# Performance work log

Hardware: AMD Instinct MI355X
Metric: run time of the kernel (lower is better)

## Reference

```python
import jax, jax.numpy as jnp
import numpy as np
import math

B, S, D = 4, 1024, 4096
H, KVH, HD = 32, 8, 128  # n_heads, n_kv_heads, dim_per_head
MAXB, MAXS = 4, 4096
START_POS = 1024


def setup_inputs() -> dict:
    key = jax.random.key(0)
    ks = jax.random.split(key, 7)
    scale = 0.02
    return {
        "x": jax.random.normal(ks[0], (B, S, D), dtype=jnp.float32),
        "wq": jax.random.normal(ks[1], (D, H * HD), dtype=jnp.float32) * scale,
        "wk": jax.random.normal(ks[2], (D, KVH * HD), dtype=jnp.float32) * scale,
        "wv": jax.random.normal(ks[3], (D, KVH * HD), dtype=jnp.float32) * scale,
        "wo": jax.random.normal(ks[4], (H * HD, D), dtype=jnp.float32) * scale,
        # cache positions [0, START_POS) hold previous context k/v
        "cache_k": jax.random.normal(ks[5], (MAXB, MAXS, KVH, HD), dtype=jnp.float32),
        "cache_v": jax.random.normal(ks[6], (MAXB, MAXS, KVH, HD), dtype=jnp.float32),
        "start_pos": START_POS,
    }


def _apply_rope(t, start_pos):
    # t: [B, S, n_heads, HD]; rotate interleaved (even, odd) pairs.
    hd = t.shape[-1]
    inv_freq = 1.0 / (10000.0 ** (jnp.arange(0, hd, 2, dtype=jnp.float32) / hd))
    m = jnp.arange(start_pos, start_pos + t.shape[1], dtype=jnp.float32)
    freqs = m[:, None] * inv_freq[None, :]              # [S, HD/2]
    cos = jnp.cos(freqs)[None, :, None, :]
    sin = jnp.sin(freqs)[None, :, None, :]
    tr = t.astype(jnp.float32).reshape(*t.shape[:-1], hd // 2, 2)
    a, b = tr[..., 0], tr[..., 1]
    out = jnp.stack([a * cos - b * sin, a * sin + b * cos], axis=-1)
    out = out.reshape(t.shape).astype(t.dtype)
    # original torch code runs RoPE under no_grad -> detached output
    return jax.lax.stop_gradient(out)


def reference(x, wq, wk, wv, wo, cache_k, cache_v, start_pos):
    b, s, d = x.shape
    kvh, hd = cache_k.shape[2], cache_k.shape[3]
    h = wq.shape[1] // hd
    n_rep = h // kvh

    xq = (x @ wq).reshape(b, s, h, hd)
    xk = (x @ wk).reshape(b, s, kvh, hd)
    xv = (x @ wv).reshape(b, s, kvh, hd)

    xq = _apply_rope(xq, start_pos)
    xk = _apply_rope(xk, start_pos)

    # KV-cache append
    cache_k = jax.lax.dynamic_update_slice(cache_k, xk, (0, start_pos, 0, 0))
    cache_v = jax.lax.dynamic_update_slice(cache_v, xv, (0, start_pos, 0, 0))
    keys = cache_k[:b, : start_pos + s]    # [B, T, KVH, HD]
    values = cache_v[:b, : start_pos + s]

    # GQA attention without materializing repeated K/V: group q heads by kv head
    q = xq.reshape(b, s, kvh, n_rep, hd)
    scores = jnp.einsum("bsgrh,btgh->bgrst", q, keys) / math.sqrt(hd)
    attn = jax.nn.softmax(scores.astype(jnp.float32), axis=-1).astype(xq.dtype)
    out = jnp.einsum("bgrst,btgh->bsgrh", attn, values).reshape(b, s, h * hd)
    return out @ wo
```

## Files before the change

### kernel.cpp

```cpp
#include <hip/hip_runtime.h>

typedef unsigned short u16;
typedef unsigned int u32;
typedef __bf16 bf16x8 __attribute__((ext_vector_type(8)));
typedef float f32x4 __attribute__((ext_vector_type(4)));
typedef u16 u16x4 __attribute__((ext_vector_type(4)));

#define B_ 4
#define S_ 1024
#define D_ 4096
#define H_ 32
#define KVH_ 8
#define HD_ 128
#define NTOK (B_*S_)
#define TTOT 2048
#define STARTP 1024

__device__ __forceinline__ float b2f(u16 x){ u32 u = ((u32)x) << 16; return __builtin_bit_cast(float, u); }
__device__ __forceinline__ u16 f2b(float f){
  u32 u = __builtin_bit_cast(u32, f);
  u32 r = (u + 0x7fffu + ((u >> 16) & 1u)) >> 16;
  return (u16)r;
}

__device__ __forceinline__ void gl2lds16(const u16* g, u16* l){
  __builtin_amdgcn_global_load_lds(
      (const __attribute__((address_space(1))) u32*)g,
      (__attribute__((address_space(3))) u32*)l, 16, 0, 0);
}

template <typename OT>
__global__ __launch_bounds__(256) void gemm_bt(const u16* __restrict__ A,
                                               const u16* __restrict__ BT,
                                               OT* __restrict__ C,
                                               int M, int N, int K)
{
  __shared__ __align__(16) u16 lA[128*32];
  __shared__ __align__(16) u16 lB[128*32];
  const int tid  = threadIdx.x;
  const int wave = tid >> 6, lane = tid & 63;
  const int q4 = lane >> 4, l15 = lane & 15;
  const int m0 = blockIdx.y * 128, n0 = blockIdx.x * 128;
  const int wm = (wave >> 1) * 64, wn = (wave & 1) * 64;
  const int srow = tid >> 2;
  const int scol = (tid & 3) * 8;

  const u16* ga = A  + (size_t)(m0 + srow) * K + scol;
  const u16* gb = BT + (size_t)(n0 + srow) * K + scol;

  f32x4 acc[4][4];
  #pragma unroll
  for (int i = 0; i < 4; i++)
    #pragma unroll
    for (int j = 0; j < 4; j++) acc[i][j] = (f32x4){0.f, 0.f, 0.f, 0.f};

  for (int k0 = 0; k0 < K; k0 += 32) {
    __builtin_amdgcn_s_waitcnt(0);
    __syncthreads();
    gl2lds16(ga + k0,                 &lA[tid * 8]);
    gl2lds16(ga + k0 + (size_t)64*K,  &lA[2048 + tid * 8]);
    gl2lds16(gb + k0,                 &lB[tid * 8]);
    gl2lds16(gb + k0 + (size_t)64*K,  &lB[2048 + tid * 8]);
    __builtin_amdgcn_s_waitcnt(0);
    __syncthreads();

    bf16x8 af[4], bb[4];
    #pragma unroll
    for (int mt = 0; mt < 4; mt++)
      af[mt] = *(const bf16x8*)&lA[(wm + mt*16 + l15) * 32 + q4 * 8];
    #pragma unroll
    for (int nt = 0; nt < 4; nt++)
      bb[nt] = *(const bf16x8*)&lB[(wn + nt*16 + l15) * 32 + q4 * 8];
    #pragma unroll
    for (int mt = 0; mt < 4; mt++)
      #pragma unroll
      for (int nt = 0; nt < 4; nt++)
        acc[mt][nt] = __builtin_amdgcn_mfma_f32_16x16x32_bf16(af[mt], bb[nt], acc[mt][nt], 0, 0, 0);
  }

  #pragma unroll
  for (int mt = 0; mt < 4; mt++) {
    #pragma unroll
    for (int r = 0; r < 4; r++) {
      int row = m0 + wm + mt*16 + q4*4 + r;
      OT* crow = C + (size_t)row * N + n0 + wn + l15;
      #pragma unroll
      for (int nt = 0; nt < 4; nt++) {
        if constexpr (sizeof(OT) == 2) crow[nt * 16] = f2b(acc[mt][nt][r]);
        else                           crow[nt * 16] = acc[mt][nt][r];
      }
    }
  }
}

__global__ __launch_bounds__(256) void cvt(const float* __restrict__ in,
                                           u16* __restrict__ out, int n)
{
  int i = (blockIdx.x * 256 + threadIdx.x) * 4;
  if (i >= n) return;
  float4 v = *(const float4*)(in + i);
  u16x4 o; o[0]=f2b(v.x); o[1]=f2b(v.y); o[2]=f2b(v.z); o[3]=f2b(v.w);
  *(u16x4*)(out + i) = o;
}

__global__ __launch_bounds__(256) void cvt_transpose(const float* __restrict__ in,
                                                     u16* __restrict__ out,
                                                     int R, int C)
{
  __shared__ u16 t[64][65];
  const int c0 = blockIdx.x * 64, r0 = blockIdx.y * 64;
  const int tid = threadIdx.x;
  const int lr = tid >> 4;
  const int lc = (tid & 15) * 4;
  #pragma unroll
  for (int i = 0; i < 4; i++) {
    int r = lr + i * 16;
    float4 v = *(const float4*)&in[(size_t)(r0 + r) * C + c0 + lc];
    t[r][lc] = f2b(v.x); t[r][lc+1] = f2b(v.y); t[r][lc+2] = f2b(v.z); t[r][lc+3] = f2b(v.w);
  }
  __syncthreads();
  #pragma unroll
  for (int i = 0; i < 4; i++) {
    int r = lr + i * 16;
    u16x4 v;
    v[0] = t[lc][r]; v[1] = t[lc+1][r]; v[2] = t[lc+2][r]; v[3] = t[lc+3][r];
    *(u16x4*)&out[(size_t)(c0 + r) * R + r0 + lc] = v;
  }
}

__global__ __launch_bounds__(256) void build_k(const float* __restrict__ ck,
                                               const u16* __restrict__ xk,
                                               u16* __restrict__ kall)
{
  int i = (blockIdx.x * 256 + threadIdx.x) * 4;
  const int hd = i & 127;
  const int t  = (i >> 7) & 2047;
  const int g  = (i >> 18) & 7;
  const int b  = i >> 21;
  u16x4 o;
  if (t < 1024) {
    const float* src = ck + ((size_t)(b * 4096 + t) * 8 + g) * 128 + hd;
    float4 v = *(const float4*)src;
    o[0]=f2b(v.x); o[1]=f2b(v.y); o[2]=f2b(v.z); o[3]=f2b(v.w);
  } else {
    const u16* src = xk + (size_t)(b * 1024 + (t - 1024)) * 1024 + g * 128 + hd;
    o = *(const u16x4*)src;
  }
  *(u16x4*)(kall + i) = o;
}

__global__ __launch_bounds__(256) void build_vt(const float* __restrict__ cv,
                                                const u16* __restrict__ xv,
                                                u16* __restrict__ vT)
{
  __shared__ u16 t[64][65];
  const int id = blockIdx.x;
  const int ht = id & 1;
  const int tt = (id >> 1) & 31;
  const int g  = (id >> 6) & 7;
  const int b  = id >> 9;
  const int t0 = tt * 64, hd0 = ht * 64;
  const int tid = threadIdx.x;
  const int lr = tid >> 4, lc = (tid & 15) * 4;
  if (t0 < 1024) {
    const float* base = cv + ((size_t)(b * 4096 + t0) * 8 + g) * 128 + hd0;
    #pragma unroll
    for (int i = 0; i < 4; i++) {
      int r = lr + i * 16;
      float4 v = *(const float4*)&base[(size_t)r * 1024 + lc];
      t[r][lc] = f2b(v.x); t[r][lc+1] = f2b(v.y); t[r][lc+2] = f2b(v.z); t[r][lc+3] = f2b(v.w);
    }
  } else {
    const u16* base = xv + (size_t)(b * 1024 + (t0 - 1024)) * 1024 + g * 128 + hd0;
    #pragma unroll
    for (int i = 0; i < 4; i++) {
      int r = lr + i * 16;
      u16x4 v = *(const u16x4*)&base[(size_t)r * 1024 + lc];
      t[r][lc] = v[0]; t[r][lc+1] = v[1]; t[r][lc+2] = v[2]; t[r][lc+3] = v[3];
    }
  }
  __syncthreads();
  u16* obase = vT + ((size_t)((b * 8 + g) * 128 + hd0)) * 2048 + t0;
  #pragma unroll
  for (int i = 0; i < 4; i++) {
    int r = lr + i * 16;
    u16x4 v;
    v[0] = t[lc][r]; v[1] = t[lc+1][r]; v[2] = t[lc+2][r]; v[3] = t[lc+3][r];
    *(u16x4*)&obase[(size_t)r * 2048 + lc] = v;
  }
}

__global__ __launch_bounds__(256) void rope(u16* __restrict__ x, int nh)
{
  const int idx = blockIdx.x * 256 + threadIdx.x;
  const int total = NTOK * nh * 64;
  if (idx >= total) return;
  const int i  = idx & 63;
  const int hh = (idx >> 6) % nh;
  const int tk = idx / (64 * nh);
  const int s  = tk & (S_ - 1);
  const float m = (float)(STARTP + s);
  const float freq = m * exp2f(-(float)(2 * i) * (13.287712379549449f / 128.0f));
  const float cs = cosf(freq), sn = sinf(freq);
  size_t off = (size_t)tk * (nh * 128) + hh * 128 + 2 * i;
  float a = b2f(x[off]), b = b2f(x[off + 1]);
  x[off]     = f2b(a * cs - b * sn);
  x[off + 1] = f2b(a * sn + b * cs);
}

__global__ __launch_bounds__(1024) void attn(const u16* __restrict__ xq,
                                             const u16* __restrict__ kall,
                                             const u16* __restrict__ vT,
                                             u16* __restrict__ out)
{
  __shared__ __align__(16) u16 lK[2][64 * 128];
  __shared__ __align__(16) u16 lV[2][128 * 64];
  __shared__ __align__(16) u16 lP[16][16][32];

  const int tid = threadIdx.x;
  const int w = tid >> 6, lane = tid & 63;
  const int q4 = lane >> 4, l15 = lane & 15;
  const int st = blockIdx.x, g = blockIdx.y, b = blockIdx.z;
  const int h = g * 4 + (w & 3);
  const int srow = st * 64 + (w >> 2) * 16;

  const u16* qrow = xq + ((size_t)(b * S_ + srow + l15) * (H_ * HD_) + h * HD_) + q4 * 8;
  bf16x8 qf[4];
  #pragma unroll
  for (int kk = 0; kk < 4; kk++) qf[kk] = *(const bf16x8*)(qrow + kk * 32);

  f32x4 o[8];
  #pragma unroll
  for (int i = 0; i < 8; i++) o[i] = (f32x4){0.f, 0.f, 0.f, 0.f};
  float ls[4] = {0.f, 0.f, 0.f, 0.f};

  const u16* kb = kall + (size_t)(b * KVH_ + g) * TTOT * HD_;
  const u16* vb = vT   + (size_t)(b * KVH_ + g) * HD_ * TTOT;

  const int rk = tid >> 4;
  const int ckb = (tid & 15) << 4;
  const u16* gK = kb + (size_t)rk * HD_ + ((ckb ^ ((rk & 7) << 4)) >> 1);
  const int rv = tid >> 3;
  const int cvb = (tid & 7) << 4;
  const u16* gV = vb + (size_t)rv * TTOT + ((cvb ^ ((rv & 7) << 4)) >> 1);

  u16* dK[2] = { &lK[0][0] + tid * 8, &lK[1][0] + tid * 8 };
  u16* dV[2] = { &lV[0][0] + tid * 8, &lV[1][0] + tid * 8 };

  u16 (*pw)[32] = lP[w];
  const float SC = 0.12751936438002815f;
  const int xk0 = (l15 & 7) << 4;
  (void)xk0;

  gl2lds16(gK, dK[0]);
  gl2lds16(gV, dV[0]);
  asm volatile("s_waitcnt vmcnt(0)" ::: "memory");
  __syncthreads();

  for (int t0 = 0; t0 < TTOT; t0 += 64) {
    const int cur = (t0 >> 6) & 1;
    if (t0 + 64 < TTOT) {
      gl2lds16(gK + (size_t)(t0 + 64) * HD_, dK[cur ^ 1]);
      gl2lds16(gV + (t0 + 64),               dV[cur ^ 1]);
    }
    const u16* K0 = &lK[cur][0];
    const u16* V0 = &lV[cur][0];

    #pragma unroll
    for (int c = 0; c < 2; c++) {
      const int r0 = c * 32 + l15;
      const int xr = (r0 & 7) << 4;
      f32x4 s0 = (f32x4){0.f,0.f,0.f,0.f}, s1 = (f32x4){0.f,0.f,0.f,0.f};
      #pragma unroll
      for (int kk = 0; kk < 4; kk++) {
        const int cb = ((kk << 6) + (q4 << 4)) ^ xr;
        bf16x8 k0 = *(const bf16x8*)(K0 + r0 * 128 + (cb >> 1));
        bf16x8 k1 = *(const bf16x8*)(K0 + (r0 + 16) * 128 + (cb >> 1));
        s0 = __builtin_amdgcn_mfma_f32_16x16x32_bf16(qf[kk], k0, s0, 0, 0, 0);
        s1 = __builtin_amdgcn_mfma_f32_16x16x32_bf16(qf[kk], k1, s1, 0, 0, 0);
      }
      float p0[4], p1[4];
      #pragma unroll
      for (int r = 0; r < 4; r++) { p0[r] = exp2f(s0[r] * SC); p1[r] = exp2f(s1[r] * SC); }
      #pragma unroll
      for (int r = 0; r < 4; r++) {
        ls[r] += p0[r] + p1[r];
        pw[q4 * 4 + r][l15]      = f2b(p0[r]);
        pw[q4 * 4 + r][16 + l15] = f2b(p1[r]);
      }
      asm volatile("s_waitcnt lgkmcnt(0)" ::: "memory");
      bf16x8 pf = *(const bf16x8*)&pw[l15][q4 * 8];
      const int xv2 = (l15 & 7) << 4;
      #pragma unroll
      for (int nt = 0; nt < 8; nt++) {
        const int rvv = nt * 16 + l15;
        const int cb = ((c << 6) + (q4 << 4)) ^ xv2;
        bf16x8 vf = *(const bf16x8*)(V0 + rvv * 64 + (cb >> 1));
        o[nt] = __builtin_amdgcn_mfma_f32_16x16x32_bf16(pf, vf, o[nt], 0, 0, 0);
      }
    }

    asm volatile("s_waitcnt vmcnt(0)" ::: "memory");
    __syncthreads();
  }

  #pragma unroll
  for (int r = 0; r < 4; r++) {
    #pragma unroll
    for (int m = 1; m < 16; m <<= 1) ls[r] += __shfl_xor(ls[r], m, 64);
    ls[r] = 1.0f / ls[r];
  }
  #pragma unroll
  for (int r = 0; r < 4; r++) {
    u16* orow = out + (size_t)(b * S_ + srow + q4 * 4 + r) * (H_ * HD_) + h * HD_ + l15;
    #pragma unroll
    for (int nt = 0; nt < 8; nt++)
      orow[nt * 16] = f2b(o[nt][r] * ls[r]);
  }
}

extern "C" void kernel_launch(void* const* d_in, const int* in_sizes, int n_in,
                              void* d_out, int out_size, void* d_ws, size_t ws_size,
                              hipStream_t stream)
{
  (void)in_sizes; (void)n_in; (void)out_size; (void)ws_size;
  const float* x  = (const float*)d_in[0];
  const float* wq = (const float*)d_in[1];
  const float* wk = (const float*)d_in[2];
  const float* wv = (const float*)d_in[3];
  const float* wo = (const float*)d_in[4];
  const float* ck = (const float*)d_in[5];
  const float* cv = (const float*)d_in[6];

  u16* ws  = (u16*)d_ws;
  u16* wqT = ws;
  u16* wkT = wqT + 16777216;
  u16* wvT = wkT + 4194304;
  u16* woT = wvT + 4194304;
  u16* xb  = woT + 16777216;
  u16* xq  = xb  + 16777216;
  u16* xk  = xq  + 16777216;
  u16* xv  = xk  + 4194304;
  u16* kall= xv  + 4194304;
  u16* vT  = kall+ 8388608;
  u16* ao  = xb;

  cvt_transpose<<<dim3(64, 64), 256, 0, stream>>>(wq, wqT, 4096, 4096);
  cvt_transpose<<<dim3(16, 64), 256, 0, stream>>>(wk, wkT, 4096, 1024);
  cvt_transpose<<<dim3(16, 64), 256, 0, stream>>>(wv, wvT, 4096, 1024);
  cvt_transpose<<<dim3(64, 64), 256, 0, stream>>>(wo, woT, 4096, 4096);
  cvt<<<16384, 256, 0, stream>>>(x, xb, 16777216);

  gemm_bt<u16><<<dim3(32, 32), 256, 0, stream>>>(xb, wqT, xq, 4096, 4096, 4096);
  gemm_bt<u16><<<dim3(8, 32),  256, 0, stream>>>(xb, wkT, xk, 4096, 1024, 4096);
  gemm_bt<u16><<<dim3(8, 32),  256, 0, stream>>>(xb, wvT, xv, 4096, 1024, 4096);

  rope<<<32768, 256, 0, stream>>>(xq, 32);
  rope<<<8192, 256, 0, stream>>>(xk, 8);

  build_k<<<8192, 256, 0, stream>>>(ck, xk, kall);
  build_vt<<<2048, 256, 0, stream>>>(cv, xv, vT);

  attn<<<dim3(16, 8, 4), 1024, 0, stream>>>(xq, kall, vT, ao);

  gemm_bt<float><<<dim3(32, 32), 256, 0, stream>>>(ao, woT, (float*)d_out, 4096, 4096, 4096);
}
```

Before: 1.164 ms.

## Add 256x256 ping-pong pipelined GEMM for Q and output projections

After: 1.006 ms. 13.6% less time.

```diff
diff --git a/kernel.cpp b/kernel.cpp
--- a/kernel.cpp
+++ b/kernel.cpp
@@ -27,6 +27,187 @@
   __builtin_amdgcn_global_load_lds(
       (const __attribute__((address_space(1))) u32*)g,
       (__attribute__((address_space(3))) u32*)l, 16, 0, 0);
+}
+
+__device__ __forceinline__ void pbar(){
+  __builtin_amdgcn_sched_barrier(0);
+  __builtin_amdgcn_s_barrier();
+  __builtin_amdgcn_sched_barrier(0);
+}
+
+template<int J, int DB>
+__device__ __forceinline__ void stage256(const u16* g, size_t rowK64, int kof,
+                                         u16* lds, int tid)
+{
+  constexpr int slot = (J==0) ? 0 : (J==3) ? 1 : (J==1) ? 2 : 3;
+  u16* d = lds + DB*32768 + slot*8192 + tid*8;
+  gl2lds16(g + kof, d);
+  gl2lds16(g + kof + rowK64, d + 4096);
+}
+
+template<int D, int MH>
+__device__ __forceinline__ void lda_half(const u16* lds, int wm, int l15,
+                                         int q4, int xr, bf16x8 (&a)[4][2])
+{
+  const u16* Ab = lds + D*32768 + wm*8192;
+  #pragma unroll
+  for (int fi = 0; fi < 4; fi++) {
+    const int r = (MH*4 + fi)*16 + l15;
+    #pragma unroll
+    for (int ks = 0; ks < 2; ks++)
+      a[fi][ks] = *(const bf16x8*)(Ab + r*64 + (((ks*64 + q4*16) ^ xr) >> 1));
+  }
+}
+
+template<int D, int NH>
+__device__ __forceinline__ void ldb_half(const u16* lds, int bhalf, int browbase,
+                                         int l15, int q4, int xr, bf16x8 (&b)[4][2])
+{
+  const u16* Bb = lds + D*32768 + (2 + bhalf)*8192;
+  #pragma unroll
+  for (int ei = 0; ei < 2; ei++) {
+    const int r = browbase + (NH*2 + ei)*16 + l15;
+    #pragma unroll
+    for (int ks = 0; ks < 2; ks++)
+      b[NH*2+ei][ks] = *(const bf16x8*)(Bb + r*64 + (((ks*64 + q4*16) ^ xr) >> 1));
+  }
+}
+
+template<int MH, int NH>
+__device__ __forceinline__ void mfma_quad(const bf16x8 (&a)[4][2],
+                                          const bf16x8 (&b)[4][2],
+                                          f32x4 (&acc)[8][4])
+{
+  __builtin_amdgcn_s_setprio(1);
+  #pragma unroll
+  for (int ks = 0; ks < 2; ks++)
+    #pragma unroll
+    for (int fi = 0; fi < 4; fi++)
+      #pragma unroll
+      for (int ei = 0; ei < 2; ei++)
+        acc[MH*4+fi][NH*2+ei] = __builtin_amdgcn_mfma_f32_16x16x32_bf16(
+            a[fi][ks], b[NH*2+ei][ks], acc[MH*4+fi][NH*2+ei], 0, 0, 0);
+  __builtin_amdgcn_s_setprio(0);
+}
+
+template<int D>
+__device__ __forceinline__ void tile4(u16* lds,
+    const u16* gA0, const u16* gA1, const u16* gB0, const u16* gB1,
+    size_t rowK64, int k1, int k2, int tid, int wm, int bhalf, int browbase,
+    int l15, int q4, int xr,
+    bf16x8 (&a)[4][2], bf16x8 (&b)[4][2], f32x4 (&acc)[8][4])
+{
+  lda_half<D,0>(lds, wm, l15, q4, xr, a);
+  ldb_half<D,0>(lds, bhalf, browbase, l15, q4, xr, b);
+  stage256<3, D^1>(gA1, rowK64, k1, lds, tid);
+  pbar();
+  mfma_quad<0,0>(a, b, acc);
+  pbar();
+  ldb_half<D,1>(lds, bhalf, browbase, l15, q4, xr, b);
+  pbar();
+  mfma_quad<0,1>(a, b, acc);
+  pbar();
+  lda_half<D,1>(lds, wm, l15, q4, xr, a);
+  stage256<1, D>(gB0, rowK64, k2, lds, tid);
+  pbar();
+  mfma_quad<1,0>(a, b, acc);
+  pbar();
+  stage256<2, D>(gB1, rowK64, k2, lds, tid);
+  stage256<0, D>(gA0, rowK64, k2, lds, tid);
+  pbar();
+  mfma_quad<1,1>(a, b, acc);
+  __builtin_amdgcn_sched_barrier(0);
+  asm volatile("s_waitcnt vmcnt(6)" ::: "memory");
+  __builtin_amdgcn_sched_barrier(0);
+  __builtin_amdgcn_s_barrier();
+  __builtin_amdgcn_sched_barrier(0);
+}
+
+template <typename OT>
+__global__ __launch_bounds__(512, 2) void gemm256(const u16* __restrict__ A,
+                                                  const u16* __restrict__ BT,
+                                                  OT* __restrict__ C,
+                                                  int M, int N, int K)
+{
+  __shared__ __align__(16) u16 lds[65536];
+  const int tid = threadIdx.x;
+  const int wave = tid >> 6, lane = tid & 63;
+  const int q4 = lane >> 4, l15 = lane & 15;
+  const int wm = wave >> 2, wn = wave & 3;
+  const int bhalf = wn >> 1;
+  const int browbase = (wn & 1) * 64;
+  const int xr = (l15 & 7) << 4;
+
+  const int nbx = N >> 8;
+  const int nwg = (M >> 8) * nbx;
+  const int cpx = nwg >> 3;
+  const int bid = (int)blockIdx.x;
+  const int swz = (bid & 7) * cpx + (bid >> 3);
+  const int bm0 = (swz / nbx) << 8;
+  const int bn0 = (swz % nbx) << 8;
+
+  const int nt = K >> 6;
+  const int ntm1 = nt - 1;
+
+  const int rb = tid >> 3;
+  const int c_off = ((((tid & 7) ^ (rb & 7)) << 4) >> 1);
+  const size_t rowK64 = (size_t)64 * K;
+  const u16* gA0 = A + (size_t)(bm0 + rb) * K + c_off;
+  const u16* gA1 = gA0 + (size_t)128 * K;
+  const u16* gB0 = BT + (size_t)(bn0 + rb) * K + c_off;
+  const u16* gB1 = gB0 + (size_t)128 * K;
+
+  bf16x8 a[4][2], b[4][2];
+  f32x4 acc[8][4];
+  #pragma unroll
+  for (int i = 0; i < 8; i++)
+    #pragma unroll
+    for (int j = 0; j < 4; j++) acc[i][j] = (f32x4){0.f, 0.f, 0.f, 0.f};
+
+  stage256<0,0>(gA0, rowK64, 0, lds, tid);
+  stage256<1,0>(gB0, rowK64, 0, lds, tid);
+  stage256<2,0>(gB1, rowK64, 0, lds, tid);
+  stage256<3,0>(gA1, rowK64, 0, lds, tid);
+  stage256<0,1>(gA0, rowK64, 64, lds, tid);
+  stage256<1,1>(gB0, rowK64, 64, lds, tid);
+  stage256<2,1>(gB1, rowK64, 64, lds, tid);
+  asm volatile("s_waitcnt vmcnt(6)" ::: "memory");
+  __builtin_amdgcn_sched_barrier(0);
+  __builtin_amdgcn_s_barrier();
+  __builtin_amdgcn_sched_barrier(0);
+
+  for (int t = 0; t < nt; t += 2) {
+    {
+      const int k1 = (t+1 < ntm1 ? t+1 : ntm1) * 64;
+      const int k2 = (t+2 < ntm1 ? t+2 : ntm1) * 64;
+      tile4<0>(lds, gA0, gA1, gB0, gB1, rowK64, k1, k2, tid, wm, bhalf,
+               browbase, l15, q4, xr, a, b, acc);
+    }
+    {
+      const int k1 = (t+2 < ntm1 ? t+2 : ntm1) * 64;
+      const int k2 = (t+3 < ntm1 ? t+3 : ntm1) * 64;
+      tile4<1>(lds, gA0, gA1, gB0, gB1, rowK64, k1, k2, tid, wm, bhalf,
+               browbase, l15, q4, xr, a, b, acc);
+    }
+  }
+
+  __builtin_amdgcn_sched_barrier(0);
+  asm volatile("s_waitcnt vmcnt(0)" ::: "memory");
+  __builtin_amdgcn_sched_barrier(0);
+
+  #pragma unroll
+  for (int f = 0; f < 8; f++) {
+    #pragma unroll
+    for (int r = 0; r < 4; r++) {
+      const int row = bm0 + wm*128 + f*16 + q4*4 + r;
+      OT* crow = C + (size_t)row * N + bn0 + wn*64 + l15;
+      #pragma unroll
+      for (int e = 0; e < 4; e++) {
+        if constexpr (sizeof(OT) == 2) crow[e*16] = f2b(acc[f][e][r]);
+        else                           crow[e*16] = acc[f][e][r];
+      }
+    }
+  }
 }
 
 template <typename OT>
@@ -249,8 +430,6 @@
 
   u16 (*pw)[32] = lP[w];
   const float SC = 0.12751936438002815f;
-  const int xk0 = (l15 & 7) << 4;
-  (void)xk0;
 
   gl2lds16(gK, dK[0]);
   gl2lds16(gV, dV[0]);
@@ -351,7 +530,7 @@
   cvt_transpose<<<dim3(64, 64), 256, 0, stream>>>(wo, woT, 4096, 4096);
   cvt<<<16384, 256, 0, stream>>>(x, xb, 16777216);
 
-  gemm_bt<u16><<<dim3(32, 32), 256, 0, stream>>>(xb, wqT, xq, 4096, 4096, 4096);
+  gemm256<u16><<<dim3(256), 512, 0, stream>>>(xb, wqT, xq, 4096, 4096, 4096);
   gemm_bt<u16><<<dim3(8, 32),  256, 0, stream>>>(xb, wkT, xk, 4096, 1024, 4096);
   gemm_bt<u16><<<dim3(8, 32),  256, 0, stream>>>(xb, wvT, xv, 4096, 1024, 4096);
 
@@ -363,5 +542,5 @@
 
   attn<<<dim3(16, 8, 4), 1024, 0, stream>>>(xq, kall, vT, ao);
 
-  gemm_bt<float><<<dim3(32, 32), 256, 0, stream>>>(ao, woT, (float*)d_out, 4096, 4096, 4096);
-}
+  gemm256<float><<<dim3(256), 512, 0, stream>>>(ao, woT, (float*)d_out, 4096, 4096, 4096);
+}
```
